# Optimization experiments

Hardware: AMD Instinct MI355X
Metric: run time of the kernel (lower is better)

## Reference

```python
import jax, jax.numpy as jnp
import numpy as np

N = 50000      # nodes
E = 800000     # edges (avg degree 16)
F_IN = 128     # num_features
HID = 128      # hidden_channels
C = 40         # num_classes


def setup_inputs() -> dict:
    key = jax.random.key(0)
    ks = jax.random.split(key, 8)
    x = jax.random.normal(ks[0], (N, F_IN), dtype=jnp.float32)
    edge_index = jax.random.randint(ks[1], (2, E), 0, N, dtype=jnp.int64)
    def glorot(k, fan_in, fan_out):
        s = np.sqrt(6.0 / (fan_in + fan_out)).astype(np.float32)
        return jax.random.uniform(k, (fan_in, fan_out), jnp.float32, -s, s)
    return {
        "x": x,
        "W1": glorot(ks[2], F_IN, HID), "b1": jnp.zeros((HID,), jnp.float32),
        "W2": glorot(ks[3], HID, HID),  "b2": jnp.zeros((HID,), jnp.float32),
        "W3": glorot(ks[4], HID, C),   "b3": jnp.zeros((C,), jnp.float32),
        "edge_index": edge_index,
    }


def reference(x, W1, b1, W2, b2, W3, b3, edge_index):
    # GCN with symmetric normalization and self-loops (PyG GCNConv semantics),
    # eval mode (dropout p=0.0), log-softmax output.
    src = edge_index[0]
    dst = edge_index[1]
    loop = jnp.arange(N, dtype=edge_index.dtype)
    src = jnp.concatenate([src, loop])      # [E+N]
    dst = jnp.concatenate([dst, loop])      # [E+N]
    ew = jnp.ones((E + N,), jnp.float32)    # edge_weight=None -> ones
    # deg[i] = sum of incoming edge weights at node i (aggregation index = dst/col)
    deg = jax.ops.segment_sum(ew, dst, num_segments=N)
    dinv = jnp.where(deg > 0, jax.lax.rsqrt(deg), 0.0)
    norm = dinv[src] * ew * dinv[dst]       # [E+N]

    def conv(h, W, b):
        # linear transform first (no bias), then gather->scale->scatter-add, then bias
        m = (h @ W)[src] * norm[:, None]                      # [E+N, out]
        return jax.ops.segment_sum(m, dst, num_segments=N) + b

    h = jax.nn.relu(conv(x, W1, b1))
    h = jax.nn.relu(conv(h, W2, b2))
    h = conv(h, W3, b3)
    return jax.nn.log_softmax(h, axis=-1)
```

## Files before the change

### kernel.cpp

```cpp
#include <hip/hip_runtime.h>
#include <math.h>

#define N_NODES 50000
#define N_EDGES 800000
#define BUCKET 64
#define SCAT_BLKS 392
#define QPG 4082
#define GEMM_BLKS 196

typedef __attribute__((ext_vector_type(8))) short short8;
typedef __attribute__((ext_vector_type(4))) float f32x4;

__device__ __forceinline__ ushort f2bf(float f) {
    union { float f; uint u; } v; v.f = f;
    uint r = v.u + 0x7FFFu + ((v.u >> 16) & 1u);
    return (ushort)(r >> 16);
}
__device__ __forceinline__ float bflo(uint p) {
    union { uint u; float f; } v; v.u = p << 16; return v.f;
}
__device__ __forceinline__ float bfhi(uint p) {
    union { uint u; float f; } v; v.u = p & 0xFFFF0000u; return v.f;
}

__global__ __launch_bounds__(512) void fused_gemm1_scatter_k(
        const float* __restrict__ Af, const float* __restrict__ W, ushort* __restrict__ Y,
        const int* __restrict__ src, const int* __restrict__ dst,
        int* __restrict__ cnt, ushort* __restrict__ colb) {
    constexpr int NT = 8;
    __shared__ ushort sB[4 * NT * 64 * 8];
    const int tid = threadIdx.x;

    if (blockIdx.x < SCAT_BLKS) {
        const int r = blockIdx.x & 7;
        const int g = blockIdx.x >> 3;
        const int lo = r * 6250;
        const int4* s32 = reinterpret_cast<const int4*>(src);
        const int4* d32 = reinterpret_cast<const int4*>(dst);
        const int qbeg = g * QPG + tid;
        const int qend = min((g + 1) * QPG, N_EDGES / 4);
#pragma unroll
        for (int u = 0; u < 8; u++) {
            const int q = qbeg + u * 512;
            if (q < qend) {
                const int4 d4 = d32[q];
                const int4 s4 = s32[q];
                if ((uint)(d4.x - lo) < 6250u) {
                    int p = atomicAdd(&cnt[d4.x], 1);
                    colb[(size_t)d4.x * BUCKET + p] = (ushort)s4.x;
                }
                if ((uint)(d4.y - lo) < 6250u) {
                    int p = atomicAdd(&cnt[d4.y], 1);
                    colb[(size_t)d4.y * BUCKET + p] = (ushort)s4.y;
                }
                if ((uint)(d4.z - lo) < 6250u) {
                    int p = atomicAdd(&cnt[d4.z], 1);
                    colb[(size_t)d4.z * BUCKET + p] = (ushort)s4.z;
                }
                if ((uint)(d4.w - lo) < 6250u) {
                    int p = atomicAdd(&cnt[d4.w], 1);
                    colb[(size_t)d4.w * BUCKET + p] = (ushort)s4.w;
                }
            }
        }
        return;
    }

    constexpr int FP = NT * 16;
    for (int i = tid; i < 128 * FP; i += 512) {
        const int k = i / FP, n = i % FP;
        const int s = k >> 5, r2 = (k >> 3) & 3, j = k & 7;
        const int t = n >> 4, nl = n & 15;
        const int l = r2 * 16 + nl;
        const int lp = (l & 56) | ((l + (l >> 3)) & 7);
        sB[(((s * NT + t) * 64) + lp) * 8 + j] = f2bf(W[k * 128 + n]);
    }
    __syncthreads();

    const int wid = tid >> 6, lane = tid & 63;
    const int lp = (lane & 56) | ((lane + (lane >> 3)) & 7);
    const int t0 = (blockIdx.x - SCAT_BLKS) * 16 + wid * 2;
    const int t1 = t0 + 1;
    const int t0c = min(t0, N_NODES / 16 - 1);
    const int t1c = min(t1, N_NODES / 16 - 1);

    f32x4 acc[2][NT];
#pragma unroll
    for (int u = 0; u < 2; u++)
#pragma unroll
        for (int t = 0; t < NT; t++) acc[u][t] = (f32x4){0.f, 0.f, 0.f, 0.f};

#pragma unroll
    for (int s = 0; s < 4; s++) {
        short8 a0, a1;
        const int ko = 32 * s + 8 * (lane >> 4);
        const float4* p0 = reinterpret_cast<const float4*>(Af + (size_t)(t0c * 16 + (lane & 15)) * 128 + ko);
        const float4* p1 = reinterpret_cast<const float4*>(Af + (size_t)(t1c * 16 + (lane & 15)) * 128 + ko);
        float4 u0 = p0[0], u1 = p0[1], v0 = p1[0], v1 = p1[1];
        a0[0] = f2bf(u0.x); a0[1] = f2bf(u0.y); a0[2] = f2bf(u0.z); a0[3] = f2bf(u0.w);
        a0[4] = f2bf(u1.x); a0[5] = f2bf(u1.y); a0[6] = f2bf(u1.z); a0[7] = f2bf(u1.w);
        a1[0] = f2bf(v0.x); a1[1] = f2bf(v0.y); a1[2] = f2bf(v0.z); a1[3] = f2bf(v0.w);
        a1[4] = f2bf(v1.x); a1[5] = f2bf(v1.y); a1[6] = f2bf(v1.z); a1[7] = f2bf(v1.w);
#pragma unroll
        for (int t = 0; t < NT; t++) {
            short8 b = *reinterpret_cast<const short8*>(&sB[(((s * NT + t) * 64) + lp) * 8]);
            acc[0][t] = __builtin_amdgcn_mfma_f32_16x16x32_bf16(a0, b, acc[0][t], 0, 0, 0);
            acc[1][t] = __builtin_amdgcn_mfma_f32_16x16x32_bf16(a1, b, acc[1][t], 0, 0, 0);
        }
    }

    const int rl = 4 * (lane >> 4), cl = lane & 15;
#pragma unroll
    for (int u = 0; u < 2; u++) {
        const int tile = u ? t1 : t0;
        if (tile >= N_NODES / 16) continue;
        const int row0 = tile * 16;
#pragma unroll
        for (int t = 0; t < NT; t++) {
            const int c = 16 * t + cl;
#pragma unroll
            for (int g = 0; g < 4; g++)
                Y[(size_t)(row0 + rl + g) * 128 + c] = f2bf(acc[u][t][g]);
        }
    }
}

template <int NT>
__global__ __launch_bounds__(512) void gemm_scaled_k(const ushort* __restrict__ Ab,
                                                     const float* __restrict__ W,
                                                     const int* __restrict__ cnt,
                                                     ushort* __restrict__ Y,
                                                     const int fout) {
    __shared__ ushort sB[4 * NT * 64 * 8];
    const int tid = threadIdx.x;
    constexpr int FP = NT * 16;
    for (int i = tid; i < 128 * FP; i += 512) {
        const int k = i / FP, n = i % FP;
        const int s = k >> 5, r2 = (k >> 3) & 3, j = k & 7;
        const int t = n >> 4, nl = n & 15;
        const int l = r2 * 16 + nl;
        const int lp = (l & 56) | ((l + (l >> 3)) & 7);
        sB[(((s * NT + t) * 64) + lp) * 8 + j] = (n < fout) ? f2bf(W[k * fout + n]) : (ushort)0;
    }
    __syncthreads();

    const int wid = tid >> 6, lane = tid & 63;
    const int lp = (lane & 56) | ((lane + (lane >> 3)) & 7);
    const int t0 = blockIdx.x * 16 + wid * 2;
    const int t1 = t0 + 1;
    const int t0c = min(t0, N_NODES / 16 - 1);
    const int t1c = min(t1, N_NODES / 16 - 1);

    f32x4 acc[2][NT];
#pragma unroll
    for (int u = 0; u < 2; u++)
#pragma unroll
        for (int t = 0; t < NT; t++) acc[u][t] = (f32x4){0.f, 0.f, 0.f, 0.f};

#pragma unroll
    for (int s = 0; s < 4; s++) {
        const int ko = 32 * s + 8 * (lane >> 4);
        short8 a0 = *reinterpret_cast<const short8*>(Ab + (size_t)(t0c * 16 + (lane & 15)) * 128 + ko);
        short8 a1 = *reinterpret_cast<const short8*>(Ab + (size_t)(t1c * 16 + (lane & 15)) * 128 + ko);
#pragma unroll
        for (int t = 0; t < NT; t++) {
            short8 b = *reinterpret_cast<const short8*>(&sB[(((s * NT + t) * 64) + lp) * 8]);
            acc[0][t] = __builtin_amdgcn_mfma_f32_16x16x32_bf16(a0, b, acc[0][t], 0, 0, 0);
            acc[1][t] = __builtin_amdgcn_mfma_f32_16x16x32_bf16(a1, b, acc[1][t], 0, 0, 0);
        }
    }

    const int rl = 4 * (lane >> 4), cl = lane & 15;
#pragma unroll
    for (int u = 0; u < 2; u++) {
        const int tile = u ? t1 : t0;
        if (tile >= N_NODES / 16) continue;
        const int row0 = tile * 16;
#pragma unroll
        for (int g = 0; g < 4; g++) {
            const int row = row0 + rl + g;
            const float dr = rsqrtf((float)(cnt[row] + 1));
#pragma unroll
            for (int t = 0; t < NT; t++) {
                const int c = 16 * t + cl;
                if (NT == 3 && c >= fout) continue;
                Y[(size_t)row * fout + c] = f2bf(acc[u][t][g] * dr);
            }
        }
    }
}

__global__ __launch_bounds__(256) void gather1_k(const ushort* __restrict__ XW,
                                                 const int* __restrict__ cnt,
                                                 const ushort* __restrict__ colb,
                                                 const float* __restrict__ bias,
                                                 ushort* __restrict__ out) {
    const int node = (blockIdx.x * 256 + threadIdx.x) >> 6;
    const int lane = threadIdx.x & 63;
    if (node >= N_NODES) return;
    const int n = cnt[node];
    const float di = rsqrtf((float)(n + 1));
    int sl = 0; float wl = 0.f;
    if (lane < n) {
        sl = colb[(size_t)node * BUCKET + lane];
        wl = rsqrtf((float)(cnt[sl] + 1));
    }
    const uint* XW32 = reinterpret_cast<const uint*>(XW);

    float a0 = 0.f, a1 = 0.f, b0 = 0.f, b1 = 0.f;
    float c0 = 0.f, c1 = 0.f, d0 = 0.f, d1 = 0.f;
    int e = 0;
    for (; e + 4 <= n; e += 4) {
        const int s0 = __shfl(sl, e),     s1 = __shfl(sl, e + 1);
        const int s2 = __shfl(sl, e + 2), s3 = __shfl(sl, e + 3);
        const float w0 = __shfl(wl, e),     w1 = __shfl(wl, e + 1);
        const float w2 = __shfl(wl, e + 2), w3 = __shfl(wl, e + 3);
        const uint p0 = XW32[(size_t)s0 * 64 + lane];
        const uint p1 = XW32[(size_t)s1 * 64 + lane];
        const uint p2 = XW32[(size_t)s2 * 64 + lane];
        const uint p3 = XW32[(size_t)s3 * 64 + lane];
        a0 = fmaf(bflo(p0), w0, a0); a1 = fmaf(bfhi(p0), w0, a1);
        b0 = fmaf(bflo(p1), w1, b0); b1 = fmaf(bfhi(p1), w1, b1);
        c0 = fmaf(bflo(p2), w2, c0); c1 = fmaf(bfhi(p2), w2, c1);
        d0 = fmaf(bflo(p3), w3, d0); d1 = fmaf(bfhi(p3), w3, d1);
    }
    for (; e < n; e++) {
        const int s = __shfl(sl, e);
        const float w = __shfl(wl, e);
        const uint p = XW32[(size_t)s * 64 + lane];
        a0 = fmaf(bflo(p), w, a0); a1 = fmaf(bfhi(p), w, a1);
    }
    const uint ps = XW32[(size_t)node * 64 + lane];
    float t0 = (a0 + b0) + (c0 + d0); t0 = fmaf(bflo(ps), di, t0);
    float t1 = (a1 + b1) + (c1 + d1); t1 = fmaf(bfhi(ps), di, t1);
    const float o0 = fmaxf(fmaf(di, t0, bias[2 * lane]), 0.f);
    const float o1 = fmaxf(fmaf(di, t1, bias[2 * lane + 1]), 0.f);
    reinterpret_cast<uint*>(out)[(size_t)node * 64 + lane] =
        (uint)f2bf(o0) | ((uint)f2bf(o1) << 16);
}

__global__ __launch_bounds__(256) void gather_add_k(const ushort* __restrict__ XWn,
                                                    const int* __restrict__ cnt,
                                                    const ushort* __restrict__ colb,
                                                    const float* __restrict__ bias,
                                                    ushort* __restrict__ out) {
    const int node = (blockIdx.x * 256 + threadIdx.x) >> 6;
    const int lane = threadIdx.x & 63;
    if (node >= N_NODES) return;
    const int n = cnt[node];
    const float di = rsqrtf((float)(n + 1));
    const ushort4* bucket = reinterpret_cast<const ushort4*>(colb + (size_t)node * BUCKET);
    const uint* XW32 = reinterpret_cast<const uint*>(XWn);

    float a0 = 0.f, a1 = 0.f, b0 = 0.f, b1 = 0.f;
    float c0 = 0.f, c1 = 0.f, d0 = 0.f, d1 = 0.f;
    int e = 0;
    for (; e + 4 <= n; e += 4) {
        const ushort4 s4 = bucket[e >> 2];
        const uint p0 = XW32[(size_t)s4.x * 64 + lane];
        const uint p1 = XW32[(size_t)s4.y * 64 + lane];
        const uint p2 = XW32[(size_t)s4.z * 64 + lane];
        const uint p3 = XW32[(size_t)s4.w * 64 + lane];
        a0 += bflo(p0); a1 += bfhi(p0);
        b0 += bflo(p1); b1 += bfhi(p1);
        c0 += bflo(p2); c1 += bfhi(p2);
        d0 += bflo(p3); d1 += bfhi(p3);
    }
    for (; e < n; e++) {
        const ushort s = colb[(size_t)node * BUCKET + e];
        const uint p = XW32[(size_t)s * 64 + lane];
        a0 += bflo(p); a1 += bfhi(p);
    }
    const uint ps = XW32[(size_t)node * 64 + lane];
    const float t0 = ((a0 + b0) + (c0 + d0)) + bflo(ps);
    const float t1 = ((a1 + b1) + (c1 + d1)) + bfhi(ps);
    const float o0 = fmaxf(fmaf(di, t0, bias[2 * lane]), 0.f);
    const float o1 = fmaxf(fmaf(di, t1, bias[2 * lane + 1]), 0.f);
    reinterpret_cast<uint*>(out)[(size_t)node * 64 + lane] =
        (uint)f2bf(o0) | ((uint)f2bf(o1) << 16);
}

__global__ __launch_bounds__(256) void gather40_lsm_k(const ushort* __restrict__ XWn,
                                                      const int* __restrict__ cnt,
                                                      const ushort* __restrict__ colb,
                                                      const float* __restrict__ bias,
                                                      float* __restrict__ out) {
    const int node = (blockIdx.x * 256 + threadIdx.x) >> 6;
    const int lane = threadIdx.x & 63;
    if (node >= N_NODES) return;
    const int g = lane < 20 ? 0 : (lane < 40 ? 1 : 2);
    const int ll = lane - g * 20;
    const int llc = min(ll, 19);
    const int n = cnt[node];
    const float di = rsqrtf((float)(n + 1));
    const uint* XW32 = reinterpret_cast<const uint*>(XWn);

    float a0 = 0.f, a1 = 0.f;
    for (int e = g; e < n; e += 3) {
        const ushort s = colb[(size_t)node * BUCKET + e];
        const uint p = XW32[(size_t)s * 20 + llc];
        a0 += bflo(p); a1 += bfhi(p);
    }
    const float t1 = __shfl(a0, lane + 20), t2 = __shfl(a0, lane + 40);
    const float u1 = __shfl(a1, lane + 20), u2 = __shfl(a1, lane + 40);
    float v0 = -INFINITY, v1 = -INFINITY;
    if (lane < 20) {
        const uint ps = XW32[(size_t)node * 20 + lane];
        v0 = fmaf(di, (a0 + t1 + t2) + bflo(ps), bias[2 * lane]);
        v1 = fmaf(di, (a1 + u1 + u2) + bfhi(ps), bias[2 * lane + 1]);
    }
    float m = fmaxf(v0, v1);
#pragma unroll
    for (int o = 32; o > 0; o >>= 1) m = fmaxf(m, __shfl_xor(m, o));
    float s = (lane < 20) ? (expf(v0 - m) + expf(v1 - m)) : 0.f;
#pragma unroll
    for (int o = 32; o > 0; o >>= 1) s += __shfl_xor(s, o);
    if (lane < 20) {
        const float ls = m + logf(s);
        float2 r; r.x = v0 - ls; r.y = v1 - ls;
        reinterpret_cast<float2*>(out)[(size_t)node * 20 + lane] = r;
    }
}

extern "C" void kernel_launch(void* const* d_in, const int* in_sizes, int n_in,
                              void* d_out, int out_size, void* d_ws, size_t ws_size,
                              hipStream_t stream) {
    const float* x  = (const float*)d_in[0];
    const float* W1 = (const float*)d_in[1];
    const float* b1 = (const float*)d_in[2];
    const float* W2 = (const float*)d_in[3];
    const float* b2 = (const float*)d_in[4];
    const float* W3 = (const float*)d_in[5];
    const float* b3 = (const float*)d_in[6];
    const int* ei   = (const int*)d_in[7];
    const int* srcp = ei;
    const int* dstp = ei + N_EDGES;
    float* out = (float*)d_out;

    int*    cnt  = (int*)d_ws;
    ushort* colb = (ushort*)(cnt + 50176);
    ushort* B0   = colb + (size_t)N_NODES * BUCKET;
    ushort* B1   = B0 + (size_t)N_NODES * 128;

    const int NB_W = (N_NODES * 64) / 256;

    hipMemsetAsync(cnt, 0, 50176 * sizeof(int), stream);
    fused_gemm1_scatter_k<<<SCAT_BLKS + GEMM_BLKS, 512, 0, stream>>>(
        x, W1, B1, srcp, dstp, cnt, colb);
    gather1_k<<<NB_W, 256, 0, stream>>>(B1, cnt, colb, b1, B0);
    gemm_scaled_k<8><<<GEMM_BLKS, 512, 0, stream>>>(B0, W2, cnt, B1, 128);
    gather_add_k<<<NB_W, 256, 0, stream>>>(B1, cnt, colb, b2, B0);
    gemm_scaled_k<3><<<GEMM_BLKS, 512, 0, stream>>>(B0, W3, cnt, B1, 40);
    gather40_lsm_k<<<NB_W, 256, 0, stream>>>(B1, cnt, colb, b3, out);
}
```

Baseline: 263.3 us.

## Split 128-wide gather into feature partitions with edge-parallel lanes; prescale layer-1 rows

Replaces the two 128-feature gather kernels with one kernel launched over a 2D grid. Each wavefront handles 16 packed feature pairs of one node, and its four 16-lane groups walk different edges before a cross-lane shuffle reduction. Layer 1 now calls a separate row-scaling kernel that premultiplies XW by the source degree normalization, so both layers share the unweighted gather. The intent is more parallelism and independent loads per node. The cost is an extra pass over the layer-1 activations, an extra bf16 rounding, and four times as many wavefronts each re-reading count and bucket data with narrower 64-byte row segments.

```diff
diff --git a/kernel.cpp b/kernel.cpp
--- a/kernel.cpp
+++ b/kernel.cpp
@@ -125,6 +125,20 @@
     }
 }
 
+__global__ __launch_bounds__(256) void scale_rows_k(ushort* __restrict__ B,
+                                                    const int* __restrict__ cnt) {
+    const int idx = blockIdx.x * 256 + threadIdx.x;
+    if (idx >= N_NODES * 16) return;
+    const float di = rsqrtf((float)(cnt[idx >> 4] + 1));
+    uint4 v = reinterpret_cast<uint4*>(B)[idx];
+    uint4 o;
+    o.x = (uint)f2bf(bflo(v.x) * di) | ((uint)f2bf(bfhi(v.x) * di) << 16);
+    o.y = (uint)f2bf(bflo(v.y) * di) | ((uint)f2bf(bfhi(v.y) * di) << 16);
+    o.z = (uint)f2bf(bflo(v.z) * di) | ((uint)f2bf(bfhi(v.z) * di) << 16);
+    o.w = (uint)f2bf(bflo(v.w) * di) | ((uint)f2bf(bfhi(v.w) * di) << 16);
+    reinterpret_cast<uint4*>(B)[idx] = o;
+}
+
 template <int NT>
 __global__ __launch_bounds__(512) void gemm_scaled_k(const ushort* __restrict__ Ab,
                                                      const float* __restrict__ W,
@@ -190,94 +204,53 @@
     }
 }
 
-__global__ __launch_bounds__(256) void gather1_k(const ushort* __restrict__ XW,
-                                                 const int* __restrict__ cnt,
-                                                 const ushort* __restrict__ colb,
-                                                 const float* __restrict__ bias,
-                                                 ushort* __restrict__ out) {
-    const int node = (blockIdx.x * 256 + threadIdx.x) >> 6;
-    const int lane = threadIdx.x & 63;
+__global__ __launch_bounds__(256) void gather_fp_k(const ushort* __restrict__ XWn,
+                                                   const int* __restrict__ cnt,
+                                                   const ushort* __restrict__ colb,
+                                                   const float* __restrict__ bias,
+                                                   ushort* __restrict__ out) {
+    const int wid = threadIdx.x >> 6, lane = threadIdx.x & 63;
+    const int node = blockIdx.x * 4 + wid;
+    const int p = blockIdx.y;
     if (node >= N_NODES) return;
     const int n = cnt[node];
     const float di = rsqrtf((float)(n + 1));
-    int sl = 0; float wl = 0.f;
-    if (lane < n) {
-        sl = colb[(size_t)node * BUCKET + lane];
-        wl = rsqrtf((float)(cnt[sl] + 1));
-    }
-    const uint* XW32 = reinterpret_cast<const uint*>(XW);
+    const int g = lane >> 4;
+    const int fl = lane & 15;
+    const int fo = p * 16 + fl;
+    const uint* XW32 = reinterpret_cast<const uint*>(XWn);
+    const ushort* bkt = colb + (size_t)node * BUCKET;
 
     float a0 = 0.f, a1 = 0.f, b0 = 0.f, b1 = 0.f;
     float c0 = 0.f, c1 = 0.f, d0 = 0.f, d1 = 0.f;
-    int e = 0;
-    for (; e + 4 <= n; e += 4) {
-        const int s0 = __shfl(sl, e),     s1 = __shfl(sl, e + 1);
-        const int s2 = __shfl(sl, e + 2), s3 = __shfl(sl, e + 3);
-        const float w0 = __shfl(wl, e),     w1 = __shfl(wl, e + 1);
-        const float w2 = __shfl(wl, e + 2), w3 = __shfl(wl, e + 3);
-        const uint p0 = XW32[(size_t)s0 * 64 + lane];
-        const uint p1 = XW32[(size_t)s1 * 64 + lane];
-        const uint p2 = XW32[(size_t)s2 * 64 + lane];
-        const uint p3 = XW32[(size_t)s3 * 64 + lane];
-        a0 = fmaf(bflo(p0), w0, a0); a1 = fmaf(bfhi(p0), w0, a1);
-        b0 = fmaf(bflo(p1), w1, b0); b1 = fmaf(bfhi(p1), w1, b1);
-        c0 = fmaf(bflo(p2), w2, c0); c1 = fmaf(bfhi(p2), w2, c1);
-        d0 = fmaf(bflo(p3), w3, d0); d1 = fmaf(bfhi(p3), w3, d1);
-    }
-    for (; e < n; e++) {
-        const int s = __shfl(sl, e);
-        const float w = __shfl(wl, e);
-        const uint p = XW32[(size_t)s * 64 + lane];
-        a0 = fmaf(bflo(p), w, a0); a1 = fmaf(bfhi(p), w, a1);
-    }
-    const uint ps = XW32[(size_t)node * 64 + lane];
-    float t0 = (a0 + b0) + (c0 + d0); t0 = fmaf(bflo(ps), di, t0);
-    float t1 = (a1 + b1) + (c1 + d1); t1 = fmaf(bfhi(ps), di, t1);
-    const float o0 = fmaxf(fmaf(di, t0, bias[2 * lane]), 0.f);
-    const float o1 = fmaxf(fmaf(di, t1, bias[2 * lane + 1]), 0.f);
-    reinterpret_cast<uint*>(out)[(size_t)node * 64 + lane] =
-        (uint)f2bf(o0) | ((uint)f2bf(o1) << 16);
-}
-
-__global__ __launch_bounds__(256) void gather_add_k(const ushort* __restrict__ XWn,
-                                                    const int* __restrict__ cnt,
-                                                    const ushort* __restrict__ colb,
-                                                    const float* __restrict__ bias,
-                                                    ushort* __restrict__ out) {
-    const int node = (blockIdx.x * 256 + threadIdx.x) >> 6;
-    const int lane = threadIdx.x & 63;
-    if (node >= N_NODES) return;
-    const int n = cnt[node];
-    const float di = rsqrtf((float)(n + 1));
-    const ushort4* bucket = reinterpret_cast<const ushort4*>(colb + (size_t)node * BUCKET);
-    const uint* XW32 = reinterpret_cast<const uint*>(XWn);
-
-    float a0 = 0.f, a1 = 0.f, b0 = 0.f, b1 = 0.f;
-    float c0 = 0.f, c1 = 0.f, d0 = 0.f, d1 = 0.f;
-    int e = 0;
-    for (; e + 4 <= n; e += 4) {
-        const ushort4 s4 = bucket[e >> 2];
-        const uint p0 = XW32[(size_t)s4.x * 64 + lane];
-        const uint p1 = XW32[(size_t)s4.y * 64 + lane];
-        const uint p2 = XW32[(size_t)s4.z * 64 + lane];
-        const uint p3 = XW32[(size_t)s4.w * 64 + lane];
+    int e = g;
+    for (; e + 12 < n; e += 16) {
+        const int s0 = bkt[e], s1 = bkt[e + 4], s2 = bkt[e + 8], s3 = bkt[e + 12];
+        const uint p0 = XW32[(size_t)s0 * 64 + fo];
+        const uint p1 = XW32[(size_t)s1 * 64 + fo];
+        const uint p2 = XW32[(size_t)s2 * 64 + fo];
+        const uint p3 = XW32[(size_t)s3 * 64 + fo];
         a0 += bflo(p0); a1 += bfhi(p0);
         b0 += bflo(p1); b1 += bfhi(p1);
         c0 += bflo(p2); c1 += bfhi(p2);
         d0 += bflo(p3); d1 += bfhi(p3);
     }
-    for (; e < n; e++) {
-        const ushort s = colb[(size_t)node * BUCKET + e];
-        const uint p = XW32[(size_t)s * 64 + lane];
-        a0 += bflo(p); a1 += bfhi(p);
-    }
-    const uint ps = XW32[(size_t)node * 64 + lane];
-    const float t0 = ((a0 + b0) + (c0 + d0)) + bflo(ps);
-    const float t1 = ((a1 + b1) + (c1 + d1)) + bfhi(ps);
-    const float o0 = fmaxf(fmaf(di, t0, bias[2 * lane]), 0.f);
-    const float o1 = fmaxf(fmaf(di, t1, bias[2 * lane + 1]), 0.f);
-    reinterpret_cast<uint*>(out)[(size_t)node * 64 + lane] =
-        (uint)f2bf(o0) | ((uint)f2bf(o1) << 16);
+    for (; e < n; e += 4) {
+        const int s0 = bkt[e];
+        const uint p0 = XW32[(size_t)s0 * 64 + fo];
+        a0 += bflo(p0); a1 += bfhi(p0);
+    }
+    a0 = (a0 + b0) + (c0 + d0);
+    a1 = (a1 + b1) + (c1 + d1);
+    a0 += __shfl_xor(a0, 16); a0 += __shfl_xor(a0, 32);
+    a1 += __shfl_xor(a1, 16); a1 += __shfl_xor(a1, 32);
+    if (g == 0) {
+        const uint ps = XW32[(size_t)node * 64 + fo];
+        const float o0 = fmaxf(fmaf(di, a0 + bflo(ps), bias[32 * p + 2 * fl]), 0.f);
+        const float o1 = fmaxf(fmaf(di, a1 + bfhi(ps), bias[32 * p + 2 * fl + 1]), 0.f);
+        reinterpret_cast<uint*>(out)[(size_t)node * 64 + fo] =
+            (uint)f2bf(o0) | ((uint)f2bf(o1) << 16);
+    }
 }
 
 __global__ __launch_bounds__(256) void gather40_lsm_k(const ushort* __restrict__ XWn,
@@ -347,9 +320,10 @@
     hipMemsetAsync(cnt, 0, 50176 * sizeof(int), stream);
     fused_gemm1_scatter_k<<<SCAT_BLKS + GEMM_BLKS, 512, 0, stream>>>(
         x, W1, B1, srcp, dstp, cnt, colb);
-    gather1_k<<<NB_W, 256, 0, stream>>>(B1, cnt, colb, b1, B0);
+    scale_rows_k<<<3125, 256, 0, stream>>>(B1, cnt);
+    gather_fp_k<<<dim3(12500, 4), 256, 0, stream>>>(B1, cnt, colb, b1, B0);
     gemm_scaled_k<8><<<GEMM_BLKS, 512, 0, stream>>>(B0, W2, cnt, B1, 128);
-    gather_add_k<<<NB_W, 256, 0, stream>>>(B1, cnt, colb, b2, B0);
+    gather_fp_k<<<dim3(12500, 4), 256, 0, stream>>>(B1, cnt, colb, b2, B0);
     gemm_scaled_k<3><<<GEMM_BLKS, 512, 0, stream>>>(B0, W3, cnt, B1, 40);
     gather40_lsm_k<<<NB_W, 256, 0, stream>>>(B1, cnt, colb, b3, out);
 }
```

After: 369.2 us. 40.2% more time.

## Fuse aggregation with next-layer matvec via LDS weights, drop separate GEMM kernels

Applied to the files above, without the earlier changes.

The layer-1 and layer-2 gather kernels now also apply the next layer's weight matrix per node. Each wave holds one node's aggregated row and broadcasts it by shuffle, multiplying against bf16 weights staged in shared memory. This removes the two standalone MFMA GEMM launches and the round trip of the intermediate activations through global memory. In exchange, each block re-stages W into LDS, and the per-node matvec runs on scalar FMAs instead of MFMA, which adds many shuffles and LDS reads per node. The final gather is also unrolled by two.

```diff
diff --git a/kernel.cpp b/kernel.cpp
--- a/kernel.cpp
+++ b/kernel.cpp
@@ -125,79 +125,22 @@
     }
 }
 
-template <int NT>
-__global__ __launch_bounds__(512) void gemm_scaled_k(const ushort* __restrict__ Ab,
-                                                     const float* __restrict__ W,
-                                                     const int* __restrict__ cnt,
-                                                     ushort* __restrict__ Y,
-                                                     const int fout) {
-    __shared__ ushort sB[4 * NT * 64 * 8];
+__global__ __launch_bounds__(512) void gmv2_k(const ushort* __restrict__ XW,
+                                              const int* __restrict__ cnt,
+                                              const ushort* __restrict__ colb,
+                                              const float* __restrict__ bias,
+                                              const float* __restrict__ W2,
+                                              ushort* __restrict__ out) {
+    __shared__ uint sW[128 * 64];
     const int tid = threadIdx.x;
-    constexpr int FP = NT * 16;
-    for (int i = tid; i < 128 * FP; i += 512) {
-        const int k = i / FP, n = i % FP;
-        const int s = k >> 5, r2 = (k >> 3) & 3, j = k & 7;
-        const int t = n >> 4, nl = n & 15;
-        const int l = r2 * 16 + nl;
-        const int lp = (l & 56) | ((l + (l >> 3)) & 7);
-        sB[(((s * NT + t) * 64) + lp) * 8 + j] = (n < fout) ? f2bf(W[k * fout + n]) : (ushort)0;
+    for (int i = tid; i < 128 * 64; i += 512) {
+        const int k = i >> 6, c = i & 63;
+        sW[i] = (uint)f2bf(W2[k * 128 + 2 * c]) | ((uint)f2bf(W2[k * 128 + 2 * c + 1]) << 16);
     }
     __syncthreads();
 
     const int wid = tid >> 6, lane = tid & 63;
-    const int lp = (lane & 56) | ((lane + (lane >> 3)) & 7);
-    const int t0 = blockIdx.x * 16 + wid * 2;
-    const int t1 = t0 + 1;
-    const int t0c = min(t0, N_NODES / 16 - 1);
-    const int t1c = min(t1, N_NODES / 16 - 1);
-
-    f32x4 acc[2][NT];
-#pragma unroll
-    for (int u = 0; u < 2; u++)
-#pragma unroll
-        for (int t = 0; t < NT; t++) acc[u][t] = (f32x4){0.f, 0.f, 0.f, 0.f};
-
-#pragma unroll
-    for (int s = 0; s < 4; s++) {
-        const int ko = 32 * s + 8 * (lane >> 4);
-        short8 a0 = *reinterpret_cast<const short8*>(Ab + (size_t)(t0c * 16 + (lane & 15)) * 128 + ko);
-        short8 a1 = *reinterpret_cast<const short8*>(Ab + (size_t)(t1c * 16 + (lane & 15)) * 128 + ko);
-#pragma unroll
-        for (int t = 0; t < NT; t++) {
-            short8 b = *reinterpret_cast<const short8*>(&sB[(((s * NT + t) * 64) + lp) * 8]);
-            acc[0][t] = __builtin_amdgcn_mfma_f32_16x16x32_bf16(a0, b, acc[0][t], 0, 0, 0);
-            acc[1][t] = __builtin_amdgcn_mfma_f32_16x16x32_bf16(a1, b, acc[1][t], 0, 0, 0);
-        }
-    }
-
-    const int rl = 4 * (lane >> 4), cl = lane & 15;
-#pragma unroll
-    for (int u = 0; u < 2; u++) {
-        const int tile = u ? t1 : t0;
-        if (tile >= N_NODES / 16) continue;
-        const int row0 = tile * 16;
-#pragma unroll
-        for (int g = 0; g < 4; g++) {
-            const int row = row0 + rl + g;
-            const float dr = rsqrtf((float)(cnt[row] + 1));
-#pragma unroll
-            for (int t = 0; t < NT; t++) {
-                const int c = 16 * t + cl;
-                if (NT == 3 && c >= fout) continue;
-                Y[(size_t)row * fout + c] = f2bf(acc[u][t][g] * dr);
-            }
-        }
-    }
-}
-
-__global__ __launch_bounds__(256) void gather1_k(const ushort* __restrict__ XW,
-                                                 const int* __restrict__ cnt,
-                                                 const ushort* __restrict__ colb,
-                                                 const float* __restrict__ bias,
-                                                 ushort* __restrict__ out) {
-    const int node = (blockIdx.x * 256 + threadIdx.x) >> 6;
-    const int lane = threadIdx.x & 63;
-    if (node >= N_NODES) return;
+    const int node = blockIdx.x * 8 + wid;
     const int n = cnt[node];
     const float di = rsqrtf((float)(n + 1));
     int sl = 0; float wl = 0.f;
@@ -233,20 +176,39 @@
     const uint ps = XW32[(size_t)node * 64 + lane];
     float t0 = (a0 + b0) + (c0 + d0); t0 = fmaf(bflo(ps), di, t0);
     float t1 = (a1 + b1) + (c1 + d1); t1 = fmaf(bfhi(ps), di, t1);
-    const float o0 = fmaxf(fmaf(di, t0, bias[2 * lane]), 0.f);
-    const float o1 = fmaxf(fmaf(di, t1, bias[2 * lane + 1]), 0.f);
+    const float h0 = fmaxf(fmaf(di, t0, bias[2 * lane]), 0.f);
+    const float h1v = fmaxf(fmaf(di, t1, bias[2 * lane + 1]), 0.f);
+
+    float o0 = 0.f, o1 = 0.f;
+#pragma unroll
+    for (int i = 0; i < 64; i++) {
+        const float hk0 = __shfl(h0, i);
+        const float hk1 = __shfl(h1v, i);
+        const uint wa = sW[(2 * i) * 64 + lane];
+        const uint wb = sW[(2 * i + 1) * 64 + lane];
+        o0 = fmaf(hk0, bflo(wa), o0); o1 = fmaf(hk0, bfhi(wa), o1);
+        o0 = fmaf(hk1, bflo(wb), o0); o1 = fmaf(hk1, bfhi(wb), o1);
+    }
     reinterpret_cast<uint*>(out)[(size_t)node * 64 + lane] =
-        (uint)f2bf(o0) | ((uint)f2bf(o1) << 16);
-}
-
-__global__ __launch_bounds__(256) void gather_add_k(const ushort* __restrict__ XWn,
-                                                    const int* __restrict__ cnt,
-                                                    const ushort* __restrict__ colb,
-                                                    const float* __restrict__ bias,
-                                                    ushort* __restrict__ out) {
-    const int node = (blockIdx.x * 256 + threadIdx.x) >> 6;
-    const int lane = threadIdx.x & 63;
-    if (node >= N_NODES) return;
+        (uint)f2bf(o0 * di) | ((uint)f2bf(o1 * di) << 16);
+}
+
+__global__ __launch_bounds__(512) void gmv3_k(const ushort* __restrict__ XWn,
+                                              const int* __restrict__ cnt,
+                                              const ushort* __restrict__ colb,
+                                              const float* __restrict__ bias,
+                                              const float* __restrict__ W3,
+                                              ushort* __restrict__ out) {
+    __shared__ uint sW[128 * 20];
+    const int tid = threadIdx.x;
+    for (int i = tid; i < 128 * 20; i += 512) {
+        const int k = i / 20, c = i % 20;
+        sW[i] = (uint)f2bf(W3[k * 40 + 2 * c]) | ((uint)f2bf(W3[k * 40 + 2 * c + 1]) << 16);
+    }
+    __syncthreads();
+
+    const int wid = tid >> 6, lane = tid & 63;
+    const int node = blockIdx.x * 8 + wid;
     const int n = cnt[node];
     const float di = rsqrtf((float)(n + 1));
     const ushort4* bucket = reinterpret_cast<const ushort4*>(colb + (size_t)node * BUCKET);
@@ -274,10 +236,23 @@
     const uint ps = XW32[(size_t)node * 64 + lane];
     const float t0 = ((a0 + b0) + (c0 + d0)) + bflo(ps);
     const float t1 = ((a1 + b1) + (c1 + d1)) + bfhi(ps);
-    const float o0 = fmaxf(fmaf(di, t0, bias[2 * lane]), 0.f);
-    const float o1 = fmaxf(fmaf(di, t1, bias[2 * lane + 1]), 0.f);
-    reinterpret_cast<uint*>(out)[(size_t)node * 64 + lane] =
-        (uint)f2bf(o0) | ((uint)f2bf(o1) << 16);
+    const float h0 = fmaxf(fmaf(di, t0, bias[2 * lane]), 0.f);
+    const float h1v = fmaxf(fmaf(di, t1, bias[2 * lane + 1]), 0.f);
+
+    float o0 = 0.f, o1 = 0.f;
+    const int cl = min(lane, 19);
+#pragma unroll
+    for (int i = 0; i < 64; i++) {
+        const float hk0 = __shfl(h0, i);
+        const float hk1 = __shfl(h1v, i);
+        const uint wa = sW[(2 * i) * 20 + cl];
+        const uint wb = sW[(2 * i + 1) * 20 + cl];
+        o0 = fmaf(hk0, bflo(wa), o0); o1 = fmaf(hk0, bfhi(wa), o1);
+        o0 = fmaf(hk1, bflo(wb), o0); o1 = fmaf(hk1, bfhi(wb), o1);
+    }
+    if (lane < 20)
+        reinterpret_cast<uint*>(out)[(size_t)node * 20 + lane] =
+            (uint)f2bf(o0 * di) | ((uint)f2bf(o1 * di) << 16);
 }
 
 __global__ __launch_bounds__(256) void gather40_lsm_k(const ushort* __restrict__ XWn,
@@ -294,13 +269,23 @@
     const int n = cnt[node];
     const float di = rsqrtf((float)(n + 1));
     const uint* XW32 = reinterpret_cast<const uint*>(XWn);
-
-    float a0 = 0.f, a1 = 0.f;
-    for (int e = g; e < n; e += 3) {
-        const ushort s = colb[(size_t)node * BUCKET + e];
+    const ushort* bkt = colb + (size_t)node * BUCKET;
+
+    float a0 = 0.f, a1 = 0.f, b0 = 0.f, b1 = 0.f;
+    int e = g;
+    for (; e + 3 < n; e += 6) {
+        const ushort s0 = bkt[e], s1 = bkt[e + 3];
+        const uint p0 = XW32[(size_t)s0 * 20 + llc];
+        const uint p1 = XW32[(size_t)s1 * 20 + llc];
+        a0 += bflo(p0); a1 += bfhi(p0);
+        b0 += bflo(p1); b1 += bfhi(p1);
+    }
+    for (; e < n; e += 3) {
+        const ushort s = bkt[e];
         const uint p = XW32[(size_t)s * 20 + llc];
         a0 += bflo(p); a1 += bfhi(p);
     }
+    a0 += b0; a1 += b1;
     const float t1 = __shfl(a0, lane + 20), t2 = __shfl(a0, lane + 40);
     const float u1 = __shfl(a1, lane + 20), u2 = __shfl(a1, lane + 40);
     float v0 = -INFINITY, v1 = -INFINITY;
@@ -347,9 +332,7 @@
     hipMemsetAsync(cnt, 0, 50176 * sizeof(int), stream);
     fused_gemm1_scatter_k<<<SCAT_BLKS + GEMM_BLKS, 512, 0, stream>>>(
         x, W1, B1, srcp, dstp, cnt, colb);
-    gather1_k<<<NB_W, 256, 0, stream>>>(B1, cnt, colb, b1, B0);
-    gemm_scaled_k<8><<<GEMM_BLKS, 512, 0, stream>>>(B0, W2, cnt, B1, 128);
-    gather_add_k<<<NB_W, 256, 0, stream>>>(B1, cnt, colb, b2, B0);
-    gemm_scaled_k<3><<<GEMM_BLKS, 512, 0, stream>>>(B0, W3, cnt, B1, 40);
+    gmv2_k<<<6250, 512, 0, stream>>>(B1, cnt, colb, b1, W2, B0);
+    gmv3_k<<<6250, 512, 0, stream>>>(B0, cnt, colb, b2, W3, B1);
     gather40_lsm_k<<<NB_W, 256, 0, stream>>>(B1, cnt, colb, b3, out);
 }
```

Result: slower. 503.1 us (+91.1%).
